# Kernel optimization log

Hardware: AMD Instinct MI355X
Metric: run time of the kernel (lower is better)

Reference implementation:

```python
import jax, jax.numpy as jnp
import numpy as np

N = 100000      # user + item nodes
E = 600000      # number of edges
LATDIM = 128
HEAD = 4
HDIM = LATDIM // HEAD


def setup_inputs() -> dict:
    key = jax.random.key(0)
    ks = jax.random.split(key, 7)
    return {
        "embeds": jax.random.normal(ks[0], (N, LATDIM), dtype=jnp.float32),
        "qTrans": jax.random.normal(ks[1], (LATDIM, LATDIM), dtype=jnp.float32) * (1.0 / np.sqrt(LATDIM)),
        "kTrans": jax.random.normal(ks[2], (LATDIM, LATDIM), dtype=jnp.float32) * (1.0 / np.sqrt(LATDIM)),
        "vTrans": jax.random.normal(ks[3], (LATDIM, LATDIM), dtype=jnp.float32) * (1.0 / np.sqrt(LATDIM)),
        "filt": jax.random.normal(ks[4], (N, HEAD), dtype=jnp.float32),
        "rows": jax.random.randint(ks[5], (E,), 0, N, dtype=jnp.int32),
        "cols": jax.random.randint(ks[6], (E,), 0, N, dtype=jnp.int32),
    }


def reference(embeds, qTrans, kTrans, vTrans, filt, rows, cols):
    # gather endpoint embeddings: [E, latdim]
    rowEmbeds = embeds[rows]
    colEmbeds = embeds[cols]
    # per-edge multi-head q/k/v: [E, H, D]
    qEmbeds = (rowEmbeds @ qTrans).reshape(E, HEAD, HDIM)
    kEmbeds = (colEmbeds @ kTrans).reshape(E, HEAD, HDIM)
    vEmbeds = (colEmbeds @ vTrans).reshape(E, HEAD, HDIM)
    # per-edge per-head attention logits
    att = jnp.einsum('ehd,ehd->eh', qEmbeds, kEmbeds)
    att = jnp.clip(att, -10.0, 10.0)
    att = att + filt[cols]
    expAtt = jnp.exp(att)
    # segment softmax over destination rows
    attNorm = jax.ops.segment_sum(expAtt, rows, num_segments=N)[rows]
    att = expAtt / (attNorm + 1e-8)
    # weighted values, scatter-sum back to nodes
    resEdges = (att[:, :, None] * vEmbeds).reshape(E, LATDIM)
    resEmbeds = jax.ops.segment_sum(resEdges, rows, num_segments=N)
    return resEmbeds
```

## Files before the change

### kernel.cpp

```cpp
#include <hip/hip_runtime.h>

#define N_NODES 100000
#define E_EDGES 600000
#define LATDIM 128
#define HEAD 4
#define HDIM 32

#define SCAN_NB 98
#define NCHUNK 391
#define QKV_GRID (NCHUNK * 2)

typedef _Float16 f16x8 __attribute__((ext_vector_type(8)));
typedef float    f32x4 __attribute__((ext_vector_type(4)));

__device__ __forceinline__ unsigned f32_to_bf16_rne(float x) {
    unsigned u = __float_as_uint(x);
    u += 0x7fffu + ((u >> 16) & 1u);
    return u >> 16;
}

__global__ __launch_bounds__(256) void wprep_kernel(
    const float* __restrict__ qT, const float* __restrict__ kT,
    const float* __restrict__ vT,
    unsigned short* __restrict__ WT,
    int* __restrict__ counts, unsigned* __restrict__ state)
{
    int g = blockIdx.x * 256 + threadIdx.x;

    for (int i = g; i < N_NODES; i += SCAN_NB * 256) counts[i] = 0;
    if (g < 128) state[g] = 0u;

    if (g >= 3072) return;
    int m    = g >> 10;
    int rem  = g & 1023;
    int c    = rem >> 3;
    int k0   = (rem & 7) * 16;
    const float* W = (m == 0) ? qT : (m == 1) ? kT : vT;

    unsigned short hv[16];
    #pragma unroll
    for (int j = 0; j < 16; ++j) {
        _Float16 h = (_Float16)W[(size_t)(k0 + j) * 128 + c];
        hv[j] = __builtin_bit_cast(unsigned short, h);
    }
    size_t off = (size_t)m * 16384 + (size_t)c * 128 + k0;
    *(uint4*)(WT + off)     = *(const uint4*)&hv[0];
    *(uint4*)(WT + off + 8) = *(const uint4*)&hv[8];
}

__global__ __launch_bounds__(256) void qkv_mfma_kernel(
    const float* __restrict__ embeds,
    const unsigned short* __restrict__ WT,
    const int* __restrict__ rows,
    int* __restrict__ counts,
    float* __restrict__ Q, unsigned* __restrict__ KV)
{
    __shared__ __align__(16) char smem[49152];

    const int tid  = threadIdx.x;
    const int half = blockIdx.x & 1;
    const int chunk = blockIdx.x >> 1;

    #pragma unroll
    for (int it = 0; it < 12; ++it) {
        const int m   = it >> 2;
        const int idx = (it & 3) * 256 + tid;
        uint4 v = *(const uint4*)((const char*)(WT + (size_t)m * 16384
                                                   + (size_t)half * 8192) + idx * 16);
        int c = idx >> 4;
        int b = (c * 256 + (idx & 15) * 16) ^ ((c & 7) << 4);
        *(uint4*)(smem + m * 16384 + b) = v;
    }
    __syncthreads();

    const int lane = tid & 63;
    const int wv   = tid >> 6;
    const int lrow = lane & 15;
    const int kg   = lane >> 4;

    for (int t = 0; t < 4; ++t) {
        const int rowT = chunk * 256 + t * 64 + wv * 16;
        const int arow = rowT + lrow;
        const bool rok = arow < N_NODES;

        f16x8 a[4];
        #pragma unroll
        for (int kk = 0; kk < 4; ++kk) {
            float4 u0 = make_float4(0.f, 0.f, 0.f, 0.f), u1 = u0;
            if (rok) {
                const float* p = embeds + (size_t)arow * 128 + kk * 32 + kg * 8;
                u0 = *(const float4*)p;
                u1 = *(const float4*)(p + 4);
            }
            a[kk][0] = (_Float16)u0.x; a[kk][1] = (_Float16)u0.y;
            a[kk][2] = (_Float16)u0.z; a[kk][3] = (_Float16)u0.w;
            a[kk][4] = (_Float16)u1.x; a[kk][5] = (_Float16)u1.y;
            a[kk][6] = (_Float16)u1.z; a[kk][7] = (_Float16)u1.w;
        }

#define MFMA_M(ACC, M) do {                                                      \
        _Pragma("unroll")                                                        \
        for (int kk = 0; kk < 4; ++kk) {                                         \
            _Pragma("unroll")                                                    \
            for (int n = 0; n < 4; ++n) {                                        \
                int col  = n * 16 + lrow;                                        \
                int byte = (col * 256 + kk * 64 + kg * 16) ^ ((lrow & 7) << 4);  \
                f16x8 b = __builtin_bit_cast(f16x8,                              \
                          *(const uint4*)(smem + (M) * 16384 + byte));           \
                ACC[n] = __builtin_amdgcn_mfma_f32_16x16x32_f16(a[kk], b, ACC[n], 0, 0, 0); \
            }                                                                    \
        }                                                                        \
    } while (0)

        f32x4 kreg[4];
        {
            f32x4 acc[4] = { {0.f,0.f,0.f,0.f}, {0.f,0.f,0.f,0.f},
                             {0.f,0.f,0.f,0.f}, {0.f,0.f,0.f,0.f} };
            MFMA_M(acc, 0);
            #pragma unroll
            for (int n = 0; n < 4; ++n)
                #pragma unroll
                for (int j = 0; j < 4; ++j) {
                    int gr  = rowT + kg * 4 + j;
                    int col = half * 64 + n * 16 + lrow;
                    if (gr < N_NODES) Q[(size_t)gr * 128 + col] = acc[n][j];
                }
        }
        {
            f32x4 acc[4] = { {0.f,0.f,0.f,0.f}, {0.f,0.f,0.f,0.f},
                             {0.f,0.f,0.f,0.f}, {0.f,0.f,0.f,0.f} };
            MFMA_M(acc, 1);
            kreg[0] = acc[0]; kreg[1] = acc[1]; kreg[2] = acc[2]; kreg[3] = acc[3];
        }
        {
            f32x4 acc[4] = { {0.f,0.f,0.f,0.f}, {0.f,0.f,0.f,0.f},
                             {0.f,0.f,0.f,0.f}, {0.f,0.f,0.f,0.f} };
            MFMA_M(acc, 2);
            #pragma unroll
            for (int n = 0; n < 4; ++n)
                #pragma unroll
                for (int j = 0; j < 4; ++j) {
                    int gr  = rowT + kg * 4 + j;
                    int col = half * 64 + n * 16 + lrow;
                    if (gr < N_NODES) {
                        unsigned pk = f32_to_bf16_rne(kreg[n][j])
                                    | (f32_to_bf16_rne(acc[n][j]) << 16);
                        KV[(size_t)gr * 128 + col] = pk;
                    }
                }
        }
#undef MFMA_M
    }

    for (int e = blockIdx.x * 256 + tid; e < E_EDGES; e += QKV_GRID * 256)
        atomicAdd(&counts[rows[e]], 1);
}

__global__ __launch_bounds__(256) void scan_lb_kernel(
    const int* __restrict__ counts, int* __restrict__ starts,
    int* __restrict__ cursor, unsigned* __restrict__ state)
{
    __shared__ int s[256];
    __shared__ int bcast;
    int b = blockIdx.x, t = threadIdx.x;
    int base = b * 1024 + t * 4;
    int v0 = (base + 0 < N_NODES) ? counts[base + 0] : 0;
    int v1 = (base + 1 < N_NODES) ? counts[base + 1] : 0;
    int v2 = (base + 2 < N_NODES) ? counts[base + 2] : 0;
    int v3 = (base + 3 < N_NODES) ? counts[base + 3] : 0;
    int local = v0 + v1 + v2 + v3;
    s[t] = local;
    __syncthreads();
    for (int off = 1; off < 256; off <<= 1) {
        int x = (t >= off) ? s[t - off] : 0;
        __syncthreads();
        s[t] += x;
        __syncthreads();
    }
    int incl  = s[t];
    int excl  = incl - local;
    int total = s[255];

    if (t == 0) {
        int sum = 0;
        if (b == 0) {
            atomicExch(&state[0], ((unsigned)total << 2) | 2u);
        } else {
            atomicExch(&state[b], ((unsigned)total << 2) | 1u);
            int i = b - 1;
            while (true) {
                unsigned w = atomicAdd(&state[i], 0u);
                unsigned st = w & 3u;
                if (st == 0u) continue;
                sum += (int)(w >> 2);
                if (st == 2u) break;
                --i;
            }
            atomicExch(&state[b], ((unsigned)(sum + total) << 2) | 2u);
        }
        bcast = sum;
    }
    __syncthreads();
    int e = excl + bcast;
    if (base + 0 < N_NODES) { starts[base + 0] = e;                cursor[base + 0] = e; }
    if (base + 1 < N_NODES) { starts[base + 1] = e + v0;           cursor[base + 1] = e + v0; }
    if (base + 2 < N_NODES) { starts[base + 2] = e + v0 + v1;      cursor[base + 2] = e + v0 + v1; }
    if (base + 3 < N_NODES) { starts[base + 3] = e + v0 + v1 + v2; cursor[base + 3] = e + v0 + v1 + v2; }
}

__global__ __launch_bounds__(256) void scatter_kernel(
    const int* __restrict__ rows, const int* __restrict__ cols,
    int* __restrict__ cursor, int* __restrict__ csrCols)
{
    int e = blockIdx.x * 256 + threadIdx.x;
    if (e >= E_EDGES) return;
    int pos = atomicAdd(&cursor[rows[e]], 1);
    csrCols[pos] = cols[e];
}

__global__ __launch_bounds__(256) void att_agg_kernel(
    const float* __restrict__ Q, const unsigned* __restrict__ KV,
    const float* __restrict__ filt,
    const int* __restrict__ starts, const int* __restrict__ counts,
    const int* __restrict__ csrCols,
    float* __restrict__ out)
{
    int t = threadIdx.x;
    int node = blockIdx.x * 8 + (t >> 5);
    if (node >= N_NODES) return;
    int lane = t & 31;
    int h = lane >> 3;

    float4 q = ((const float4*)(Q + (size_t)node * 128))[lane];
    int s   = starts[node];
    int cnt = counts[node];

    float norm = 0.f;
    float ax = 0.f, ay = 0.f, az = 0.f, aw = 0.f;

    int i = 0;
    for (; i + 2 <= cnt; i += 2) {
        int c0 = csrCols[s + i];
        int c1 = csrCols[s + i + 1];
        uint4 kv0 = ((const uint4*)KV)[(size_t)c0 * 32 + lane];
        uint4 kv1 = ((const uint4*)KV)[(size_t)c1 * 32 + lane];
        float f0 = filt[c0 * HEAD + h];
        float f1 = filt[c1 * HEAD + h];

        float k0x = __uint_as_float(kv0.x << 16), v0x = __uint_as_float(kv0.x & 0xffff0000u);
        float k0y = __uint_as_float(kv0.y << 16), v0y = __uint_as_float(kv0.y & 0xffff0000u);
        float k0z = __uint_as_float(kv0.z << 16), v0z = __uint_as_float(kv0.z & 0xffff0000u);
        float k0w = __uint_as_float(kv0.w << 16), v0w = __uint_as_float(kv0.w & 0xffff0000u);
        float k1x = __uint_as_float(kv1.x << 16), v1x = __uint_as_float(kv1.x & 0xffff0000u);
        float k1y = __uint_as_float(kv1.y << 16), v1y = __uint_as_float(kv1.y & 0xffff0000u);
        float k1z = __uint_as_float(kv1.z << 16), v1z = __uint_as_float(kv1.z & 0xffff0000u);
        float k1w = __uint_as_float(kv1.w << 16), v1w = __uint_as_float(kv1.w & 0xffff0000u);

        float p0 = q.x * k0x + q.y * k0y + q.z * k0z + q.w * k0w;
        float p1 = q.x * k1x + q.y * k1y + q.z * k1z + q.w * k1w;
        p0 += __shfl_xor(p0, 1);   p1 += __shfl_xor(p1, 1);
        p0 += __shfl_xor(p0, 2);   p1 += __shfl_xor(p1, 2);
        p0 += __shfl_xor(p0, 4);   p1 += __shfl_xor(p1, 4);

        float w0 = __expf(fminf(fmaxf(p0, -10.f), 10.f) + f0);
        float w1 = __expf(fminf(fmaxf(p1, -10.f), 10.f) + f1);
        norm += w0 + w1;
        ax += w0 * v0x + w1 * v1x;
        ay += w0 * v0y + w1 * v1y;
        az += w0 * v0z + w1 * v1z;
        aw += w0 * v0w + w1 * v1w;
    }
    if (i < cnt) {
        int c0 = csrCols[s + i];
        uint4 kv0 = ((const uint4*)KV)[(size_t)c0 * 32 + lane];
        float f0 = filt[c0 * HEAD + h];
        float k0x = __uint_as_float(kv0.x << 16), v0x = __uint_as_float(kv0.x & 0xffff0000u);
        float k0y = __uint_as_float(kv0.y << 16), v0y = __uint_as_float(kv0.y & 0xffff0000u);
        float k0z = __uint_as_float(kv0.z << 16), v0z = __uint_as_float(kv0.z & 0xffff0000u);
        float k0w = __uint_as_float(kv0.w << 16), v0w = __uint_as_float(kv0.w & 0xffff0000u);
        float p0 = q.x * k0x + q.y * k0y + q.z * k0z + q.w * k0w;
        p0 += __shfl_xor(p0, 1);
        p0 += __shfl_xor(p0, 2);
        p0 += __shfl_xor(p0, 4);
        float w0 = __expf(fminf(fmaxf(p0, -10.f), 10.f) + f0);
        norm += w0;
        ax += w0 * v0x; ay += w0 * v0y; az += w0 * v0z; aw += w0 * v0w;
    }
    float inv = 1.0f / (norm + 1e-8f);
    ((float4*)(out + (size_t)node * 128))[lane] =
        make_float4(ax * inv, ay * inv, az * inv, aw * inv);
}

extern "C" void kernel_launch(void* const* d_in, const int* in_sizes, int n_in,
                              void* d_out, int out_size, void* d_ws, size_t ws_size,
                              hipStream_t stream) {
    const float* embeds = (const float*)d_in[0];
    const float* qT     = (const float*)d_in[1];
    const float* kT     = (const float*)d_in[2];
    const float* vT     = (const float*)d_in[3];
    const float* filt   = (const float*)d_in[4];
    const int*   rows   = (const int*)d_in[5];
    const int*   cols   = (const int*)d_in[6];
    float*       out    = (float*)d_out;

    float*    Q  = (float*)d_ws;
    unsigned* KV = (unsigned*)(Q + (size_t)N_NODES * 128);
    int* counts    = (int*)(KV + (size_t)N_NODES * 128);
    int* starts    = counts + N_NODES;
    int* cursor    = starts + N_NODES;
    int* csrCols   = cursor + N_NODES;
    unsigned* state = (unsigned*)(csrCols + E_EDGES);

    unsigned short* WT = (unsigned short*)csrCols;

    wprep_kernel<<<SCAN_NB, 256, 0, stream>>>(qT, kT, vT, WT, counts, state);
    qkv_mfma_kernel<<<QKV_GRID, 256, 0, stream>>>(
        embeds, WT, rows, counts, Q, KV);
    scan_lb_kernel<<<SCAN_NB, 256, 0, stream>>>(counts, starts, cursor, state);
    scatter_kernel<<<(E_EDGES + 255) / 256, 256, 0, stream>>>(rows, cols, cursor, csrCols);
    att_agg_kernel<<<(N_NODES + 7) / 8, 256, 0, stream>>>(
        Q, KV, filt, starts, counts, csrCols, out);
}
```

Baseline: 285.5 us.

## Restructure QKV projection into 64-row blocks with double-buffered weight staging

The QKV projection kernel moves from 782 blocks, each holding half of all three weight matrices in 48KB of LDS and looping over 256 rows, to 1563 blocks of 64 rows. Each block stages its embedding tile once in LDS as fp16 and streams the six weight slices through two 16KB LDS buffers, prefetching the next slice into registers while the current MFMAs run. This reads each embedding row once instead of twice (once per column half), lowers LDS use so more blocks fit per CU, and overlaps weight loads with compute, at the cost of more barriers and more total weight traffic. The attention aggregation loop is also unrolled from 2 to 4 edges to keep more gathers in flight.

```diff
diff --git a/kernel.cpp b/kernel.cpp
--- a/kernel.cpp
+++ b/kernel.cpp
@@ -7,8 +7,6 @@
 #define HDIM 32
 
 #define SCAN_NB 98
-#define NCHUNK 391
-#define QKV_GRID (NCHUNK * 2)
 
 typedef _Float16 f16x8 __attribute__((ext_vector_type(8)));
 typedef float    f32x4 __attribute__((ext_vector_type(4)));
@@ -55,105 +53,169 @@
     int* __restrict__ counts,
     float* __restrict__ Q, unsigned* __restrict__ KV)
 {
-    __shared__ __align__(16) char smem[49152];
-
-    const int tid  = threadIdx.x;
-    const int half = blockIdx.x & 1;
-    const int chunk = blockIdx.x >> 1;
-
-    #pragma unroll
-    for (int it = 0; it < 12; ++it) {
-        const int m   = it >> 2;
-        const int idx = (it & 3) * 256 + tid;
-        uint4 v = *(const uint4*)((const char*)(WT + (size_t)m * 16384
-                                                   + (size_t)half * 8192) + idx * 16);
-        int c = idx >> 4;
-        int b = (c * 256 + (idx & 15) * 16) ^ ((c & 7) << 4);
-        *(uint4*)(smem + m * 16384 + b) = v;
-    }
-    __syncthreads();
-
-    const int lane = tid & 63;
-    const int wv   = tid >> 6;
-    const int lrow = lane & 15;
-    const int kg   = lane >> 4;
-
-    for (int t = 0; t < 4; ++t) {
-        const int rowT = chunk * 256 + t * 64 + wv * 16;
-        const int arow = rowT + lrow;
-        const bool rok = arow < N_NODES;
-
-        f16x8 a[4];
-        #pragma unroll
-        for (int kk = 0; kk < 4; ++kk) {
-            float4 u0 = make_float4(0.f, 0.f, 0.f, 0.f), u1 = u0;
-            if (rok) {
-                const float* p = embeds + (size_t)arow * 128 + kk * 32 + kg * 8;
-                u0 = *(const float4*)p;
-                u1 = *(const float4*)(p + 4);
-            }
-            a[kk][0] = (_Float16)u0.x; a[kk][1] = (_Float16)u0.y;
-            a[kk][2] = (_Float16)u0.z; a[kk][3] = (_Float16)u0.w;
-            a[kk][4] = (_Float16)u1.x; a[kk][5] = (_Float16)u1.y;
-            a[kk][6] = (_Float16)u1.z; a[kk][7] = (_Float16)u1.w;
-        }
-
-#define MFMA_M(ACC, M) do {                                                      \
+    __shared__ __align__(16) char smem[32768];
+    char* R0 = smem;
+    char* R1 = smem + 16384;
+
+    const int tid = threadIdx.x;
+    const int rowBase = blockIdx.x * 64;
+
+    uint4 pb0, pb1, pb2, pb3;
+
+#define PF(MN, HN) do {                                                          \
+        const char* _s = (const char*)(WT + (size_t)(MN) * 16384                 \
+                                          + (size_t)(HN) * 8192);                \
+        pb0 = *(const uint4*)(_s + (size_t)(0 * 256 + tid) * 16);                \
+        pb1 = *(const uint4*)(_s + (size_t)(1 * 256 + tid) * 16);                \
+        pb2 = *(const uint4*)(_s + (size_t)(2 * 256 + tid) * 16);                \
+        pb3 = *(const uint4*)(_s + (size_t)(3 * 256 + tid) * 16);                \
+    } while (0)
+
+#define COMMIT(R) do {                                                           \
+        { int _i = 0 * 256 + tid; int _c = _i >> 4;                              \
+          int _s = (_c * 256 + (_i & 15) * 16) ^ ((_c & 7) << 4);                \
+          *(uint4*)((R) + _s) = pb0; }                                           \
+        { int _i = 1 * 256 + tid; int _c = _i >> 4;                              \
+          int _s = (_c * 256 + (_i & 15) * 16) ^ ((_c & 7) << 4);                \
+          *(uint4*)((R) + _s) = pb1; }                                           \
+        { int _i = 2 * 256 + tid; int _c = _i >> 4;                              \
+          int _s = (_c * 256 + (_i & 15) * 16) ^ ((_c & 7) << 4);                \
+          *(uint4*)((R) + _s) = pb2; }                                           \
+        { int _i = 3 * 256 + tid; int _c = _i >> 4;                              \
+          int _s = (_c * 256 + (_i & 15) * 16) ^ ((_c & 7) << 4);                \
+          *(uint4*)((R) + _s) = pb3; }                                           \
+    } while (0)
+
+#define MFMA_M(ACC, R) do {                                                      \
         _Pragma("unroll")                                                        \
         for (int kk = 0; kk < 4; ++kk) {                                         \
             _Pragma("unroll")                                                    \
             for (int n = 0; n < 4; ++n) {                                        \
                 int col  = n * 16 + lrow;                                        \
                 int byte = (col * 256 + kk * 64 + kg * 16) ^ ((lrow & 7) << 4);  \
-                f16x8 b = __builtin_bit_cast(f16x8,                              \
-                          *(const uint4*)(smem + (M) * 16384 + byte));           \
+                f16x8 b = __builtin_bit_cast(f16x8, *(const uint4*)((R) + byte)); \
                 ACC[n] = __builtin_amdgcn_mfma_f32_16x16x32_f16(a[kk], b, ACC[n], 0, 0, 0); \
             }                                                                    \
         }                                                                        \
     } while (0)
 
-        f32x4 kreg[4];
-        {
-            f32x4 acc[4] = { {0.f,0.f,0.f,0.f}, {0.f,0.f,0.f,0.f},
-                             {0.f,0.f,0.f,0.f}, {0.f,0.f,0.f,0.f} };
-            MFMA_M(acc, 0);
-            #pragma unroll
-            for (int n = 0; n < 4; ++n)
-                #pragma unroll
-                for (int j = 0; j < 4; ++j) {
-                    int gr  = rowT + kg * 4 + j;
-                    int col = half * 64 + n * 16 + lrow;
-                    if (gr < N_NODES) Q[(size_t)gr * 128 + col] = acc[n][j];
-                }
+#define ZACC(ACC) f32x4 ACC[4] = { {0.f,0.f,0.f,0.f}, {0.f,0.f,0.f,0.f},         \
+                                   {0.f,0.f,0.f,0.f}, {0.f,0.f,0.f,0.f} }
+
+#define STORE_Q(ACC, H) do {                                                     \
+        _Pragma("unroll")                                                        \
+        for (int n = 0; n < 4; ++n)                                              \
+        _Pragma("unroll")                                                        \
+        for (int j = 0; j < 4; ++j) {                                            \
+            int gr  = rowBase + wv * 16 + kg * 4 + j;                            \
+            int col = (H) * 64 + n * 16 + lrow;                                  \
+            if (gr < N_NODES) Q[(size_t)gr * 128 + col] = ACC[n][j];             \
+        }                                                                        \
+    } while (0)
+
+#define STORE_KV(ACC, H) do {                                                    \
+        _Pragma("unroll")                                                        \
+        for (int n = 0; n < 4; ++n)                                              \
+        _Pragma("unroll")                                                        \
+        for (int j = 0; j < 4; ++j) {                                            \
+            int gr  = rowBase + wv * 16 + kg * 4 + j;                            \
+            int col = (H) * 64 + n * 16 + lrow;                                  \
+            if (gr < N_NODES) {                                                  \
+                unsigned pk = f32_to_bf16_rne(kreg[n][j])                        \
+                            | (f32_to_bf16_rne(ACC[n][j]) << 16);                \
+                KV[(size_t)gr * 128 + col] = pk;                                 \
+            }                                                                    \
+        }                                                                        \
+    } while (0)
+
+    PF(0, 0);
+
+    #pragma unroll
+    for (int it = 0; it < 4; ++it) {
+        int idx = it * 256 + tid;
+        int r   = idx >> 4;
+        int c16 = idx & 15;
+        int gr  = rowBase + r;
+        float4 u0 = make_float4(0.f, 0.f, 0.f, 0.f), u1 = u0;
+        if (gr < N_NODES) {
+            const float* p = embeds + (size_t)gr * 128 + c16 * 8;
+            u0 = *(const float4*)p;
+            u1 = *(const float4*)(p + 4);
         }
-        {
-            f32x4 acc[4] = { {0.f,0.f,0.f,0.f}, {0.f,0.f,0.f,0.f},
-                             {0.f,0.f,0.f,0.f}, {0.f,0.f,0.f,0.f} };
-            MFMA_M(acc, 1);
-            kreg[0] = acc[0]; kreg[1] = acc[1]; kreg[2] = acc[2]; kreg[3] = acc[3];
+        f16x8 v;
+        v[0] = (_Float16)u0.x; v[1] = (_Float16)u0.y;
+        v[2] = (_Float16)u0.z; v[3] = (_Float16)u0.w;
+        v[4] = (_Float16)u1.x; v[5] = (_Float16)u1.y;
+        v[6] = (_Float16)u1.z; v[7] = (_Float16)u1.w;
+        int byte = (r * 256 + c16 * 16) ^ ((r & 7) << 4);
+        *(uint4*)(R0 + byte) = __builtin_bit_cast(uint4, v);
+    }
+    __syncthreads();
+
+    const int lane = tid & 63;
+    const int wv   = tid >> 6;
+    const int lrow = lane & 15;
+    const int kg   = lane >> 4;
+
+    f16x8 a[4];
+    {
+        const int arow = wv * 16 + lrow;
+        #pragma unroll
+        for (int kk = 0; kk < 4; ++kk) {
+            int byte = (arow * 256 + kk * 64 + kg * 16) ^ ((lrow & 7) << 4);
+            a[kk] = __builtin_bit_cast(f16x8, *(const uint4*)(R0 + byte));
         }
-        {
-            f32x4 acc[4] = { {0.f,0.f,0.f,0.f}, {0.f,0.f,0.f,0.f},
-                             {0.f,0.f,0.f,0.f}, {0.f,0.f,0.f,0.f} };
-            MFMA_M(acc, 2);
-            #pragma unroll
-            for (int n = 0; n < 4; ++n)
-                #pragma unroll
-                for (int j = 0; j < 4; ++j) {
-                    int gr  = rowT + kg * 4 + j;
-                    int col = half * 64 + n * 16 + lrow;
-                    if (gr < N_NODES) {
-                        unsigned pk = f32_to_bf16_rne(kreg[n][j])
-                                    | (f32_to_bf16_rne(acc[n][j]) << 16);
-                        KV[(size_t)gr * 128 + col] = pk;
-                    }
-                }
-        }
+    }
+    COMMIT(R1);
+    __syncthreads();
+
+    f32x4 kreg[4];
+
+    {
+        PF(1, 0); ZACC(acc);
+        MFMA_M(acc, R1);
+        STORE_Q(acc, 0);
+        COMMIT(R0); __syncthreads();
+    }
+    {
+        PF(2, 0); ZACC(acc);
+        MFMA_M(acc, R0);
+        kreg[0] = acc[0]; kreg[1] = acc[1]; kreg[2] = acc[2]; kreg[3] = acc[3];
+        COMMIT(R1); __syncthreads();
+    }
+    {
+        PF(0, 1); ZACC(acc);
+        MFMA_M(acc, R1);
+        STORE_KV(acc, 0);
+        COMMIT(R0); __syncthreads();
+    }
+    {
+        PF(1, 1); ZACC(acc);
+        MFMA_M(acc, R0);
+        STORE_Q(acc, 1);
+        COMMIT(R1); __syncthreads();
+    }
+    {
+        PF(2, 1); ZACC(acc);
+        MFMA_M(acc, R1);
+        kreg[0] = acc[0]; kreg[1] = acc[1]; kreg[2] = acc[2]; kreg[3] = acc[3];
+        COMMIT(R0); __syncthreads();
+    }
+    {
+        ZACC(acc);
+        MFMA_M(acc, R0);
+        STORE_KV(acc, 1);
+    }
+
+    for (int e = blockIdx.x * 256 + tid; e < E_EDGES; e += gridDim.x * 256)
+        atomicAdd(&counts[rows[e]], 1);
+
+#undef PF
+#undef COMMIT
 #undef MFMA_M
-    }
-
-    for (int e = blockIdx.x * 256 + tid; e < E_EDGES; e += QKV_GRID * 256)
-        atomicAdd(&counts[rows[e]], 1);
+#undef ZACC
+#undef STORE_Q
+#undef STORE_KV
 }
 
 __global__ __launch_bounds__(256) void scan_lb_kernel(
@@ -238,54 +300,48 @@
     float norm = 0.f;
     float ax = 0.f, ay = 0.f, az = 0.f, aw = 0.f;
 
+#define EDGE_BODY(KVU, F)                                                     \
+    {                                                                          \
+        float kx = __uint_as_float((KVU).x << 16), vx = __uint_as_float((KVU).x & 0xffff0000u); \
+        float ky = __uint_as_float((KVU).y << 16), vy = __uint_as_float((KVU).y & 0xffff0000u); \
+        float kz = __uint_as_float((KVU).z << 16), vz = __uint_as_float((KVU).z & 0xffff0000u); \
+        float kw = __uint_as_float((KVU).w << 16), vw = __uint_as_float((KVU).w & 0xffff0000u); \
+        float p = q.x * kx + q.y * ky + q.z * kz + q.w * kw;                   \
+        p += __shfl_xor(p, 1);                                                 \
+        p += __shfl_xor(p, 2);                                                 \
+        p += __shfl_xor(p, 4);                                                 \
+        float w = __expf(fminf(fmaxf(p, -10.f), 10.f) + (F));                  \
+        norm += w;                                                             \
+        ax += w * vx; ay += w * vy; az += w * vz; aw += w * vw;                \
+    }
+
     int i = 0;
-    for (; i + 2 <= cnt; i += 2) {
+    for (; i + 4 <= cnt; i += 4) {
         int c0 = csrCols[s + i];
         int c1 = csrCols[s + i + 1];
+        int c2 = csrCols[s + i + 2];
+        int c3 = csrCols[s + i + 3];
         uint4 kv0 = ((const uint4*)KV)[(size_t)c0 * 32 + lane];
         uint4 kv1 = ((const uint4*)KV)[(size_t)c1 * 32 + lane];
+        uint4 kv2 = ((const uint4*)KV)[(size_t)c2 * 32 + lane];
+        uint4 kv3 = ((const uint4*)KV)[(size_t)c3 * 32 + lane];
         float f0 = filt[c0 * HEAD + h];
         float f1 = filt[c1 * HEAD + h];
-
-        float k0x = __uint_as_float(kv0.x << 16), v0x = __uint_as_float(kv0.x & 0xffff0000u);
-        float k0y = __uint_as_float(kv0.y << 16), v0y = __uint_as_float(kv0.y & 0xffff0000u);
-        float k0z = __uint_as_float(kv0.z << 16), v0z = __uint_as_float(kv0.z & 0xffff0000u);
-        float k0w = __uint_as_float(kv0.w << 16), v0w = __uint_as_float(kv0.w & 0xffff0000u);
-        float k1x = __uint_as_float(kv1.x << 16), v1x = __uint_as_float(kv1.x & 0xffff0000u);
-        float k1y = __uint_as_float(kv1.y << 16), v1y = __uint_as_float(kv1.y & 0xffff0000u);
-        float k1z = __uint_as_float(kv1.z << 16), v1z = __uint_as_float(kv1.z & 0xffff0000u);
-        float k1w = __uint_as_float(kv1.w << 16), v1w = __uint_as_float(kv1.w & 0xffff0000u);
-
-        float p0 = q.x * k0x + q.y * k0y + q.z * k0z + q.w * k0w;
-        float p1 = q.x * k1x + q.y * k1y + q.z * k1z + q.w * k1w;
-        p0 += __shfl_xor(p0, 1);   p1 += __shfl_xor(p1, 1);
-        p0 += __shfl_xor(p0, 2);   p1 += __shfl_xor(p1, 2);
-        p0 += __shfl_xor(p0, 4);   p1 += __shfl_xor(p1, 4);
-
-        float w0 = __expf(fminf(fmaxf(p0, -10.f), 10.f) + f0);
-        float w1 = __expf(fminf(fmaxf(p1, -10.f), 10.f) + f1);
-        norm += w0 + w1;
-        ax += w0 * v0x + w1 * v1x;
-        ay += w0 * v0y + w1 * v1y;
-        az += w0 * v0z + w1 * v1z;
-        aw += w0 * v0w + w1 * v1w;
-    }
-    if (i < cnt) {
+        float f2 = filt[c2 * HEAD + h];
+        float f3 = filt[c3 * HEAD + h];
+        EDGE_BODY(kv0, f0);
+        EDGE_BODY(kv1, f1);
+        EDGE_BODY(kv2, f2);
+        EDGE_BODY(kv3, f3);
+    }
+    for (; i < cnt; ++i) {
         int c0 = csrCols[s + i];
         uint4 kv0 = ((const uint4*)KV)[(size_t)c0 * 32 + lane];
         float f0 = filt[c0 * HEAD + h];
-        float k0x = __uint_as_float(kv0.x << 16), v0x = __uint_as_float(kv0.x & 0xffff0000u);
-        float k0y = __uint_as_float(kv0.y << 16), v0y = __uint_as_float(kv0.y & 0xffff0000u);
-        float k0z = __uint_as_float(kv0.z << 16), v0z = __uint_as_float(kv0.z & 0xffff0000u);
-        float k0w = __uint_as_float(kv0.w << 16), v0w = __uint_as_float(kv0.w & 0xffff0000u);
-        float p0 = q.x * k0x + q.y * k0y + q.z * k0z + q.w * k0w;
-        p0 += __shfl_xor(p0, 1);
-        p0 += __shfl_xor(p0, 2);
-        p0 += __shfl_xor(p0, 4);
-        float w0 = __expf(fminf(fmaxf(p0, -10.f), 10.f) + f0);
-        norm += w0;
-        ax += w0 * v0x; ay += w0 * v0y; az += w0 * v0z; aw += w0 * v0w;
-    }
+        EDGE_BODY(kv0, f0);
+    }
+#undef EDGE_BODY
+
     float inv = 1.0f / (norm + 1e-8f);
     ((float4*)(out + (size_t)node * 128))[lane] =
         make_float4(ax * inv, ay * inv, az * inv, aw * inv);
@@ -314,7 +370,7 @@
     unsigned short* WT = (unsigned short*)csrCols;
 
     wprep_kernel<<<SCAN_NB, 256, 0, stream>>>(qT, kT, vT, WT, counts, state);
-    qkv_mfma_kernel<<<QKV_GRID, 256, 0, stream>>>(
+    qkv_mfma_kernel<<<(N_NODES + 63) / 64, 256, 0, stream>>>(
         embeds, WT, rows, counts, Q, KV);
     scan_lb_kernel<<<SCAN_NB, 256, 0, stream>>>(counts, starts, cursor, state);
     scatter_kernel<<<(E_EDGES + 255) / 256, 256, 0, stream>>>(rows, cols, cursor, csrCols);
```

Result: faster. 251.1 us (-12.0%).
